# Optimization experiments

Hardware: AMD Instinct MI355X
Metric: run time of the kernel (lower is better)

Reference implementation:

```python
import jax, jax.numpy as jnp
import numpy as np

# SMPL-like kinematic tree parents for 21 body joints (child j -> parent index in the 22-slot feature)
KTREE_PARENTS = jnp.array([0, 0, 0, 1, 2, 3, 4, 5, 6, 7, 8, 9, 9, 9, 12, 13, 14, 16, 17, 18, 19], dtype=jnp.int32)
# np.linspace(22, 64, 3, endpoint=False, dtype=int)[::-1] for num_tokens=64, token_size_div=3, num_joints+1=22
UP_SIZES = [50, 36, 22]
NUM_JOINTS_P1 = 22


def conv1d_rep(x, w, b):
    # x: (B, Cin, L), w: (Cout, Cin, 3), replicate padding of 1 on each side
    xp = jnp.pad(x, ((0, 0), (0, 0), (1, 1)), mode='edge')
    y = jax.lax.conv_general_dilated(xp, w, (1,), 'VALID', dimension_numbers=('NCH', 'OIH', 'NCH'))
    return y + b[None, :, None]


def interp_linear(x, out_size):
    # torch nn.Upsample(mode='linear', align_corners=False) semantics; x: (B, C, L)
    L = x.shape[-1]
    coords = (jnp.arange(out_size, dtype=x.dtype) + 0.5) * (L / out_size) - 0.5
    coords = jnp.clip(coords, 0.0, L - 1)
    lo = jnp.floor(coords).astype(jnp.int32)
    hi = jnp.minimum(lo + 1, L - 1)
    w = coords - lo.astype(x.dtype)
    return x[..., lo] * (1.0 - w) + x[..., hi] * w


def rotation_6d_to_matrix(d6):
    # pytorch3d convention: rows b1, b2, b3 stacked at dim=-2
    a1, a2 = d6[..., :3], d6[..., 3:]
    b1 = a1 / jnp.linalg.norm(a1, axis=-1, keepdims=True)
    a2p = a2 - jnp.sum(b1 * a2, axis=-1, keepdims=True) * b1
    b2 = a2p / jnp.linalg.norm(a2p, axis=-1, keepdims=True)
    b3 = jnp.cross(b1, b2)
    return jnp.stack([b1, b2, b3], axis=-2)


def setup_inputs() -> dict:
    key = jax.random.key(0)
    ks = jax.random.split(key, 8)
    B, T, C, W, J, D = 1024, 64, 512, 512, 21, 6
    s = 0.02
    f32 = jnp.float32
    return {
        'x': jax.random.normal(ks[0], (B, T, C), f32),
        'conv1_w': jax.random.normal(ks[1], (W, C, 3), f32) * s,
        'conv1_b': jnp.zeros((W,), f32),
        'tok_w': jax.random.normal(ks[2], (T, T), f32) * s,
        'tok_b': jnp.zeros((T,), f32),
        'up_w': jax.random.normal(ks[3], (3, W, W, 3), f32) * s,
        'up_b': jnp.zeros((3, W), f32),
        'ln_g': jnp.ones((W,), f32),
        'ln_b': jnp.zeros((W,), f32),
        'beta_w': jax.random.normal(ks[4], (W, 10), f32) * s,
        'beta_b': jnp.zeros((10,), f32),
        'pw1': jax.random.normal(ks[5], (J, 2 * W, W), f32) * s,
        'pb1': jnp.zeros((J, W), f32),
        'pw2': jax.random.normal(ks[6], (J, W, D), f32) * s,
        'pb2': jax.random.normal(ks[7], (J, D), f32) * 0.1,
    }


def reference(x, conv1_w, conv1_b, tok_w, tok_b, up_w, up_b, ln_g, ln_b,
              beta_w, beta_b, pw1, pb1, pw2, pb2):
    # ---- decoder ----
    h = x.transpose(0, 2, 1)                                   # (B, C, T)
    h = jax.nn.relu(conv1d_rep(h, conv1_w, conv1_b))            # (B, W, T)
    # Conv1d(T, T, 1) applied on token axis (after permutes) == matmul over tokens
    h = jax.nn.relu(jnp.einsum('st,bwt->bws', tok_w, h) + tok_b[None, None, :])  # (B, W, T)
    for i, sz in enumerate(UP_SIZES):
        h = conv1d_rep(interp_linear(h, sz), up_w[i], up_b[i])
        if sz != NUM_JOINTS_P1:
            h = jax.nn.relu(h)
    # h: (B, W, 22)
    m = h.mean(axis=-1)                                         # (B, W)
    mu = m.mean(-1, keepdims=True)
    var = m.var(-1, keepdims=True)
    pred_beta = ((m - mu) / jnp.sqrt(var + 1e-5) * ln_g + ln_b) @ beta_w + beta_b  # (B, 10)
    jf = h.transpose(0, 2, 1)                                   # (B, 22, W)
    curr = jf[:, 1:, :]                                         # joint j+1 feats, (B, 21, W)
    parent = jf[:, KTREE_PARENTS, :]                            # parent feats,   (B, 21, W)
    feat = jnp.concatenate([curr, parent], axis=-1)             # (B, 21, 2W)
    hid = jax.nn.relu(jnp.einsum('bjc,jch->bjh', feat, pw1) + pb1[None])
    pose6d = jnp.einsum('bjh,jhd->bjd', hid, pw2) + pb2[None]   # (B, 21, 6)
    rotmat = rotation_6d_to_matrix(pose6d)                      # (B, 21, 3, 3)
    return pose6d, rotmat, pred_beta
```

## Files before the change

### kernel.cpp

```cpp
#include <hip/hip_runtime.h>


typedef unsigned short u16;
typedef unsigned short u16x4 __attribute__((ext_vector_type(4)));
typedef unsigned short u16x8 __attribute__((ext_vector_type(8)));
typedef float f32x4 __attribute__((ext_vector_type(4)));
typedef __bf16 bf16x8 __attribute__((ext_vector_type(8)));

__constant__ int KPAR_C[21] = {0,0,0,1,2,3,4,5,6,7,8,9,9,9,12,13,14,16,17,18,19};

__device__ __forceinline__ u16 bf16rne(float v) {
  unsigned b = __builtin_bit_cast(unsigned, v);
  return (u16)((b + 0x7fffu + ((b >> 16) & 1u)) >> 16);
}
__device__ __forceinline__ float bf16tof(u16 h) {
  unsigned b = ((unsigned)h) << 16;
  return __builtin_bit_cast(float, b);
}
__device__ __forceinline__ f32x4 mfma16(u16x8 a, u16x8 b, f32x4 c) {
  return __builtin_amdgcn_mfma_f32_16x16x32_bf16(
      __builtin_bit_cast(bf16x8, a), __builtin_bit_cast(bf16x8, b), c, 0, 0, 0);
}
__device__ __forceinline__ int unpack_c(int p) {
  return (p & ~31) | (((p >> 3) & 3) << 2) | (p & 3) | ((p & 4) << 2);
}
__device__ __forceinline__ void gload_lds16(const void* g, void* l) {
  __builtin_amdgcn_global_load_lds((const __attribute__((address_space(1))) void*)g,
                                   (__attribute__((address_space(3))) void*)l, 16, 0, 0);
}

__global__ __launch_bounds__(256)
void kwprep(const float* __restrict__ conv1_w, const float* __restrict__ up_w,
            const float* __restrict__ tok_w, u16* __restrict__ WF, u16* __restrict__ TWF) {
  int idx = blockIdx.x * 256 + threadIdx.x;
  if (idx < 786432) {
    const int lane = idx & 63;
    int r = idx >> 6;
    const int nf = r & 15; r >>= 4;
    const int ks = r % 48; r /= 48;
    const int p = r & 1; r >>= 1;
    const int nh = r & 1;
    const int L = r >> 1;
    const float* Wsrc = (L == 0) ? conv1_w : (up_w + (size_t)(L - 1) * 786432);
    const int wcol = unpack_c(nh * 256 + nf * 16 + (lane & 15));
    u16x8 o;
#pragma unroll
    for (int e = 0; e < 8; ++e) {
      const int k = ks * 32 + ((lane >> 4) << 2) + (e & 3) + ((e >> 2) << 4);
      const int c = k & 511, kk = k >> 9;
      const float v = Wsrc[(size_t)wcol * 1536 + c * 3 + kk];
      const u16 h = bf16rne(v);
      o[e] = p ? bf16rne(v - bf16tof(h)) : h;
    }
    *(u16x8*)(WF + (size_t)idx * 8) = o;
  } else if (idx < 786432 + 1024) {
    const int i2 = idx - 786432;
    const int lane = i2 & 63;
    const int r = i2 >> 6;
    const int mf = r & 3;
    const int ks = (r >> 2) & 1;
    const int p = r >> 3;
    const int s = mf * 16 + (lane & 15);
    u16x8 o;
#pragma unroll
    for (int e = 0; e < 8; ++e) {
      const int t = ks * 32 + ((lane >> 4) << 2) + (e & 3) + ((e >> 2) << 4);
      const float v = tok_w[s * 64 + t];
      const u16 h = bf16rne(v);
      o[e] = p ? bf16rne(v - bf16tof(h)) : h;
    }
    *(u16x8*)(TWF + (size_t)i2 * 8) = o;
  }
}

__global__ __launch_bounds__(256)
void kpw1prep(const float* __restrict__ pw1, u16* __restrict__ PWF) {
  const int idx = blockIdx.x * 256 + threadIdx.x;
  if (idx >= 2752512) return;
  const int lane = idx & 63;
  const int nf = (idx >> 6) & 15;
  const int ks = (idx >> 10) & 31;
  const int p = (idx >> 15) & 1;
  const int nh = (idx >> 16) & 1;
  const int j = idx >> 17;
  const int w = unpack_c(nh * 256 + nf * 16 + (lane & 15));
  u16x8 o;
#pragma unroll
  for (int e = 0; e < 8; ++e) {
    const int k = ks * 32 + ((lane >> 4) << 2) + (e & 3) + ((e >> 2) << 4);
    const float v = pw1[((size_t)j * 1024 + k) * 512 + w];
    const u16 h = bf16rne(v);
    o[e] = p ? bf16rne(v - bf16tof(h)) : h;
  }
  *(u16x8*)(PWF + (size_t)idx * 8) = o;
}

template <int SLOT, int ROWS, bool SRCF32, bool F32OUT, bool RELU>
__global__ __launch_bounds__(512, 2)
void conv_gemm(const float* __restrict__ xf,
               const u16* __restrict__ ghi, const u16* __restrict__ glo,
               const u16* __restrict__ wl,
               const float* __restrict__ bias,
               u16* __restrict__ ohi, u16* __restrict__ olo,
               float* __restrict__ of32) {
  constexpr int MFW = SLOT / 16;
  constexpr int MFT = 4 * MFW;
  constexpr int ASL = (MFT + 7) / 8;
  __shared__ u16x8 Ald[2][2][MFT][64];
  __shared__ u16x8 Bld[2][2][16][64];

  const int tid = threadIdx.x, lane = tid & 63, w = tid >> 6;
  const int mw = w & 3, nw = w >> 2;
  const int nh = blockIdx.x;
  const int bb0 = blockIdx.y * 4;

  f32x4 acc[MFW][8];
#pragma unroll
  for (int m = 0; m < MFW; ++m)
#pragma unroll
    for (int n = 0; n < 8; ++n) acc[m][n] = (f32x4){0.f, 0.f, 0.f, 0.f};

  float4 sF0[ASL], sF1[ASL];

  auto STAGE = [&](int ks2, int nb) {
    if constexpr (!SRCF32) {
      const int kk2 = ks2 >> 4;
      const int pc0 = (ks2 & 15) * 32 + ((lane >> 4) << 3);
#pragma unroll
      for (int si = 0; si < ASL; ++si) {
        const int f = w + si * 8;
        if (f < MFT) {
          const int bA = f / MFW, mfA = f % MFW;
          int t = mfA * 16 + (lane & 15) - 1 + kk2;
          t = t < 0 ? 0 : (t > ROWS - 1 ? ROWS - 1 : t);
          const size_t o = ((size_t)(bb0 + bA) * ROWS + t) * 512 + pc0;
          gload_lds16(ghi + o, &Ald[nb][0][f][0]);
          gload_lds16(glo + o, &Ald[nb][1][f][0]);
        }
      }
    }
#pragma unroll
    for (int ci = 0; ci < 4; ++ci) {
      const int cch = w + ci * 8;
      const int p = cch >> 4, nf = cch & 15;
      gload_lds16(wl + ((size_t)(((nh * 2 + p) * 48 + ks2) * 16 + nf)) * 512 + lane * 8,
                  &Bld[nb][p][nf][0]);
    }
  };

  auto LOADSA = [&](int ks2) {
    const int kk2 = ks2 >> 4;
    const int c0 = (ks2 & 15) * 32 + ((lane >> 4) << 2);
#pragma unroll
    for (int si = 0; si < ASL; ++si) {
      const int f = w + si * 8;
      if (f < MFT) {
        const int bA = f / MFW, mfA = f % MFW;
        int t = mfA * 16 + (lane & 15) - 1 + kk2;
        t = t < 0 ? 0 : (t > ROWS - 1 ? ROWS - 1 : t);
        const float* src = xf + ((size_t)(bb0 + bA) * ROWS + t) * 512 + c0;
        sF0[si] = *(const float4*)src;
        sF1[si] = *(const float4*)(src + 16);
      }
    }
  };
  auto WRITESA = [&](int nb) {
#pragma unroll
    for (int si = 0; si < ASL; ++si) {
      const int f = w + si * 8;
      if (f < MFT) {
        float vv[8] = {sF0[si].x, sF0[si].y, sF0[si].z, sF0[si].w,
                       sF1[si].x, sF1[si].y, sF1[si].z, sF1[si].w};
        u16x8 hv, lv;
#pragma unroll
        for (int e = 0; e < 8; ++e) {
          const u16 h = bf16rne(vv[e]);
          hv[e] = h;
          lv[e] = bf16rne(vv[e] - bf16tof(h));
        }
        Ald[nb][0][f][lane] = hv;
        Ald[nb][1][f][lane] = lv;
      }
    }
  };

  STAGE(0, 0);
  if constexpr (SRCF32) { LOADSA(0); WRITESA(0); }
  __syncthreads();

  for (int ks = 0; ks < 48; ++ks) {
    const int buf = ks & 1;
    if (ks < 47) {
      STAGE(ks + 1, buf ^ 1);
      if constexpr (SRCF32) LOADSA(ks + 1);
    }
    u16x8 ah[MFW], al[MFW];
#pragma unroll
    for (int m = 0; m < MFW; ++m) {
      ah[m] = Ald[buf][0][mw * MFW + m][lane];
      al[m] = Ald[buf][1][mw * MFW + m][lane];
    }
    __builtin_amdgcn_s_setprio(1);
#pragma unroll
    for (int n = 0; n < 8; ++n) {
      const u16x8 bh = Bld[buf][0][nw * 8 + n][lane];
      const u16x8 bl = Bld[buf][1][nw * 8 + n][lane];
#pragma unroll
      for (int m = 0; m < MFW; ++m) {
        acc[m][n] = mfma16(ah[m], bh, acc[m][n]);
        acc[m][n] = mfma16(ah[m], bl, acc[m][n]);
        acc[m][n] = mfma16(al[m], bh, acc[m][n]);
      }
    }
    __builtin_amdgcn_s_setprio(0);
    if (ks < 47) {
      if constexpr (SRCF32) WRITESA(buf ^ 1);
    }
    __syncthreads();
  }

  const int b = bb0 + mw;
#pragma unroll
  for (int m = 0; m < MFW; ++m) {
#pragma unroll
    for (int n = 0; n < 8; ++n) {
      const int col = nh * 256 + nw * 128 + n * 16 + (lane & 15);
      const float bs = bias[unpack_c(col)];
#pragma unroll
      for (int r = 0; r < 4; ++r) {
        const int t = m * 16 + ((lane >> 4) << 2) + r;
        if (t < ROWS) {
          float v = acc[m][n][r] + bs;
          if (RELU) v = fmaxf(v, 0.f);
          const size_t o = ((size_t)b * ROWS + t) * 512 + col;
          if constexpr (F32OUT) {
            of32[o] = v;
          } else {
            const u16 h = bf16rne(v);
            ohi[o] = h;
            olo[o] = bf16rne(v - bf16tof(h));
          }
        }
      }
    }
  }
}

__global__ __launch_bounds__(512, 2)
void tok_mix(const u16* __restrict__ h1hi, const u16* __restrict__ h1lo,
             const u16* __restrict__ twf, const float* __restrict__ tok_b,
             u16* __restrict__ g1hi, u16* __restrict__ g1lo) {
  __shared__ float h1f[64][258];
  __shared__ u16x8 twl[2][2][4][64];
  __shared__ float tbl[64];
  const int tid = threadIdx.x, lane = tid & 63, w = tid >> 6;
  const int mw = w & 3, nw = w >> 2;
  const int b = blockIdx.y, ch = blockIdx.x;

  for (int i = tid; i < 1024; i += 512) ((u16x8*)twl)[i] = ((const u16x8*)twf)[i];
  if (tid < 64) tbl[tid] = tok_b[tid];
  for (int i = tid; i < 2048; i += 512) {
    const int t = i >> 5, c8 = (i & 31) * 8;
    const size_t o = ((size_t)b * 64 + t) * 512 + ch * 256 + c8;
    const u16x8 hv = *(const u16x8*)(h1hi + o);
    const u16x8 lv = *(const u16x8*)(h1lo + o);
#pragma unroll
    for (int e = 0; e < 8; ++e) h1f[t][c8 + e] = bf16tof(hv[e]) + bf16tof(lv[e]);
  }
  __syncthreads();

  f32x4 acc2[8];
#pragma unroll
  for (int n = 0; n < 8; ++n) acc2[n] = (f32x4){0.f, 0.f, 0.f, 0.f};
#pragma unroll
  for (int ksI = 0; ksI < 2; ++ksI) {
    const u16x8 ah = twl[0][ksI][mw][lane];
    const u16x8 al = twl[1][ksI][mw][lane];
    const int t0 = ksI * 32 + ((lane >> 4) << 2);
#pragma unroll
    for (int n = 0; n < 8; ++n) {
      const int c = nw * 128 + n * 16 + (lane & 15);
      u16x8 bh, bl;
#pragma unroll
      for (int e = 0; e < 8; ++e) {
        const float v = h1f[t0 + (e & 3) + ((e >> 2) << 4)][c];
        const u16 h = bf16rne(v);
        bh[e] = h;
        bl[e] = bf16rne(v - bf16tof(h));
      }
      acc2[n] = mfma16(ah, bh, acc2[n]);
      acc2[n] = mfma16(ah, bl, acc2[n]);
      acc2[n] = mfma16(al, bh, acc2[n]);
    }
  }
  __syncthreads();
#pragma unroll
  for (int n = 0; n < 8; ++n) {
    const int c = nw * 128 + n * 16 + (lane & 15);
#pragma unroll
    for (int r = 0; r < 4; ++r) {
      const int s = mw * 16 + ((lane >> 4) << 2) + r;
      h1f[s][c] = fmaxf(acc2[n][r] + tbl[s], 0.f);
    }
  }
  __syncthreads();
  const float scale = (float)(64.0 / 50.0);
  for (int i = tid; i < 50 * 256; i += 512) {
    const int s = i >> 8, c = i & 255;
    float coords = fminf(fmaxf(((float)s + 0.5f) * scale - 0.5f, 0.f), 63.f);
    const int lo = (int)floorf(coords);
    const int hi = lo + 1 < 64 ? lo + 1 : 63;
    const float wv = coords - (float)lo;
    const float v = h1f[lo][c] * (1.f - wv) + h1f[hi][c] * wv;
    const u16 h = bf16rne(v);
    const size_t o = ((size_t)b * 50 + s) * 512 + ch * 256 + c;
    g1hi[o] = h;
    g1lo[o] = bf16rne(v - bf16tof(h));
  }
}

template <int SOUT, int SIN>
__global__ __launch_bounds__(256)
void ginterp(const u16* __restrict__ ahi, const u16* __restrict__ alo,
             u16* __restrict__ ghi, u16* __restrict__ glo) {
  const int idx = blockIdx.x * 256 + threadIdx.x;
  if (idx >= 1024 * SOUT * 64) return;
  const int ch = (idx & 63) * 8;
  const int s = (idx >> 6) % SOUT;
  const int b = (idx >> 6) / SOUT;
  const float scale = (float)((double)SIN / (double)SOUT);
  float coords = fminf(fmaxf(((float)s + 0.5f) * scale - 0.5f, 0.f), (float)(SIN - 1));
  const int lo = (int)floorf(coords);
  const int hi = lo + 1 < SIN ? lo + 1 : SIN - 1;
  const float wv = coords - (float)lo;
  const size_t olo_ = ((size_t)b * SIN + lo) * 512 + ch;
  const size_t ohi_ = ((size_t)b * SIN + hi) * 512 + ch;
  const u16x8 vh0 = *(const u16x8*)(ahi + olo_), vl0 = *(const u16x8*)(alo + olo_);
  const u16x8 vh1 = *(const u16x8*)(ahi + ohi_), vl1 = *(const u16x8*)(alo + ohi_);
  u16x8 oh, ol;
#pragma unroll
  for (int e = 0; e < 8; ++e) {
    const float v0 = bf16tof(vh0[e]) + bf16tof(vl0[e]);
    const float v1 = bf16tof(vh1[e]) + bf16tof(vl1[e]);
    const float v = v0 * (1.f - wv) + v1 * wv;
    const u16 h = bf16rne(v);
    oh[e] = h;
    ol[e] = bf16rne(v - bf16tof(h));
  }
  const size_t oo = ((size_t)b * SOUT + s) * 512 + ch;
  *(u16x8*)(ghi + oo) = oh;
  *(u16x8*)(glo + oo) = ol;
}

__global__ __launch_bounds__(256)
void k_beta(const float* __restrict__ h, const float* __restrict__ ln_g,
            const float* __restrict__ ln_b, const float* __restrict__ beta_w,
            const float* __restrict__ beta_b, float* __restrict__ out) {
  __shared__ float nbuf[512];
  __shared__ float red[32];
  __shared__ float part[160];
  const int tid = threadIdx.x;
  const int b = blockIdx.x;
  const float* hb = h + (size_t)b * (22 * 512);
  float m0 = 0.f, m1 = 0.f;
  for (int t = 0; t < 22; ++t) {
    m0 += hb[t * 512 + tid];
    m1 += hb[t * 512 + tid + 256];
  }
  m0 *= (1.f / 22.f);
  m1 *= (1.f / 22.f);
  float s = m0 + m1, sq = m0 * m0 + m1 * m1;
  for (int off = 32; off > 0; off >>= 1) {
    s += __shfl_down(s, off);
    sq += __shfl_down(sq, off);
  }
  const int lane = tid & 63, wid = tid >> 6;
  if (lane == 0) { red[wid] = s; red[8 + wid] = sq; }
  __syncthreads();
  if (tid == 0) {
    float S = red[0] + red[1] + red[2] + red[3];
    float Q = red[8] + red[9] + red[10] + red[11];
    float mu = S * (1.f / 512.f);
    float var = Q * (1.f / 512.f) - mu * mu;
    red[16] = mu;
    red[17] = 1.f / sqrtf(var + 1e-5f);
  }
  __syncthreads();
  const float mu = red[16], rs = red[17];
  const int uc = unpack_c(tid);
  nbuf[tid] = (m0 - mu) * rs * ln_g[uc] + ln_b[uc];
  nbuf[tid + 256] = (m1 - mu) * rs * ln_g[uc + 256] + ln_b[uc + 256];
  __syncthreads();
  if (tid < 160) {
    const int o = tid >> 4, l = tid & 15;
    float p = 0.f;
    for (int w = l; w < 512; w += 16) p += nbuf[w] * beta_w[unpack_c(w) * 10 + o];
    part[tid] = p;
  }
  __syncthreads();
  if (tid < 10) {
    float p = beta_b[tid];
#pragma unroll
    for (int l = 0; l < 16; ++l) p += part[tid * 16 + l];
    out[(size_t)b * 10 + tid] = p;
  }
}

__global__ __launch_bounds__(512, 2)
void k_pose1(const float* __restrict__ hf, const u16* __restrict__ PWF,
             const float* __restrict__ pb1,
             u16* __restrict__ hidhi, u16* __restrict__ hidlo) {
  __shared__ u16x8 Ald[2][2][8][64];
  __shared__ u16x8 Bld[2][2][16][64];
  const int tid = threadIdx.x, lane = tid & 63, w = tid >> 6;
  const int mw = w & 1, nw = w >> 1;
  const int nh = blockIdx.x & 1, mb = blockIdx.x >> 1;
  const int j = blockIdx.y;
  const int bb0 = mb * 128;
  const int par = KPAR_C[j];
  const size_t pwbase = (size_t)(j * 2 + nh) * 524288;

  f32x4 acc[4][4];
#pragma unroll
  for (int m = 0; m < 4; ++m)
#pragma unroll
    for (int n = 0; n < 4; ++n) acc[m][n] = (f32x4){0.f, 0.f, 0.f, 0.f};

  float4 sF0, sF1;

  auto STAGE = [&](int ks, int nb) {
#pragma unroll
    for (int t = 0; t < 4; ++t) {
      const int cc = t * 8 + w;
      const int p = cc >> 4, nf = cc & 15;
      gload_lds16(PWF + pwbase + ((size_t)(p * 32 + ks) * 16 + nf) * 512 + lane * 8,
                  &Bld[nb][p][nf][0]);
    }
  };
  auto LOADSA = [&](int ks) {
    const int row = (ks < 16) ? (j + 1) : par;
    const int b = bb0 + w * 16 + (lane & 15);
    const int pc0 = (ks & 15) * 32 + ((lane >> 4) << 3);
    const float* src = hf + ((size_t)b * 22 + row) * 512 + pc0;
    sF0 = *(const float4*)src;
    sF1 = *(const float4*)(src + 4);
  };
  auto WRITESA = [&](int nb) {
    float vv[8] = {sF0.x, sF0.y, sF0.z, sF0.w, sF1.x, sF1.y, sF1.z, sF1.w};
    u16x8 hv, lv;
#pragma unroll
    for (int e = 0; e < 8; ++e) {
      const u16 h = bf16rne(vv[e]);
      hv[e] = h;
      lv[e] = bf16rne(vv[e] - bf16tof(h));
    }
    Ald[nb][0][w][lane] = hv;
    Ald[nb][1][w][lane] = lv;
  };

  STAGE(0, 0);
  LOADSA(0);
  WRITESA(0);
  __syncthreads();

  for (int ks = 0; ks < 32; ++ks) {
    const int buf = ks & 1;
    if (ks < 31) { STAGE(ks + 1, buf ^ 1); LOADSA(ks + 1); }
    u16x8 ah[4], al[4], bh[4], bl[4];
#pragma unroll
    for (int m = 0; m < 4; ++m) {
      ah[m] = Ald[buf][0][mw * 4 + m][lane];
      al[m] = Ald[buf][1][mw * 4 + m][lane];
    }
#pragma unroll
    for (int n = 0; n < 4; ++n) {
      bh[n] = Bld[buf][0][nw * 4 + n][lane];
      bl[n] = Bld[buf][1][nw * 4 + n][lane];
    }
    __builtin_amdgcn_s_setprio(1);
#pragma unroll
    for (int n = 0; n < 4; ++n)
#pragma unroll
      for (int m = 0; m < 4; ++m) {
        acc[m][n] = mfma16(ah[m], bh[n], acc[m][n]);
        acc[m][n] = mfma16(ah[m], bl[n], acc[m][n]);
        acc[m][n] = mfma16(al[m], bh[n], acc[m][n]);
      }
    __builtin_amdgcn_s_setprio(0);
    if (ks < 31) WRITESA(buf ^ 1);
    __syncthreads();
  }

#pragma unroll
  for (int m = 0; m < 4; ++m) {
#pragma unroll
    for (int n = 0; n < 4; ++n) {
      const int col = nh * 256 + nw * 64 + n * 16 + (lane & 15);
      const float bs = pb1[(size_t)j * 512 + unpack_c(col)];
#pragma unroll
      for (int r = 0; r < 4; ++r) {
        const int b = bb0 + mw * 64 + m * 16 + ((lane >> 4) << 2) + r;
        float v = fmaxf(acc[m][n][r] + bs, 0.f);
        const size_t o = ((size_t)j * 1024 + b) * 512 + col;
        const u16 h = bf16rne(v);
        hidhi[o] = h;
        hidlo[o] = bf16rne(v - bf16tof(h));
      }
    }
  }
}

__global__ __launch_bounds__(256)
void k_pose2(const u16* __restrict__ hidhi, const u16* __restrict__ hidlo,
             const float* __restrict__ pw2, const float* __restrict__ pb2,
             float* __restrict__ out) {
  __shared__ float w2l[3072];
  __shared__ float part[128 * 12];
  const int tid = threadIdx.x;
  const int mb = blockIdx.x, j = blockIdx.y;
  const int bb0 = mb * 128;
  for (int i = tid; i < 3072; i += 256) {
    const int p = i / 6, d = i - p * 6;
    w2l[i] = pw2[(size_t)j * 3072 + unpack_c(p) * 6 + d];
  }
  __syncthreads();

  const int r = tid >> 1, half = tid & 1;
  const int row = bb0 + r;
  const u16* ph = hidhi + ((size_t)j * 1024 + row) * 512 + half * 256;
  const u16* pl = hidlo + ((size_t)j * 1024 + row) * 512 + half * 256;
  float s[6] = {0.f, 0.f, 0.f, 0.f, 0.f, 0.f};
  for (int c = 0; c < 32; ++c) {
    const u16x8 hv = ((const u16x8*)ph)[c];
    const u16x8 lv = ((const u16x8*)pl)[c];
#pragma unroll
    for (int e = 0; e < 8; ++e) {
      const float v = bf16tof(hv[e]) + bf16tof(lv[e]);
      const int hidx = half * 256 + c * 8 + e;
#pragma unroll
      for (int d = 0; d < 6; ++d) s[d] = fmaf(v, w2l[hidx * 6 + d], s[d]);
    }
  }
#pragma unroll
  for (int d = 0; d < 6; ++d) part[r * 12 + half * 6 + d] = s[d];
  __syncthreads();

  if (tid < 128) {
    const int row2 = bb0 + tid;
    float p6[6];
#pragma unroll
    for (int d = 0; d < 6; ++d)
      p6[d] = part[tid * 12 + d] + part[tid * 12 + 6 + d] + pb2[j * 6 + d];
    float* po = out + ((size_t)row2 * 21 + j) * 6;
#pragma unroll
    for (int d = 0; d < 6; ++d) po[d] = p6[d];
    const float a1x = p6[0], a1y = p6[1], a1z = p6[2];
    const float a2x = p6[3], a2y = p6[4], a2z = p6[5];
    const float inv1 = 1.f / sqrtf(a1x * a1x + a1y * a1y + a1z * a1z);
    const float b1x = a1x * inv1, b1y = a1y * inv1, b1z = a1z * inv1;
    const float dot = b1x * a2x + b1y * a2y + b1z * a2z;
    const float px = a2x - dot * b1x, py = a2y - dot * b1y, pz = a2z - dot * b1z;
    const float inv2 = 1.f / sqrtf(px * px + py * py + pz * pz);
    const float b2x = px * inv2, b2y = py * inv2, b2z = pz * inv2;
    const float b3x = b1y * b2z - b1z * b2y;
    const float b3y = b1z * b2x - b1x * b2z;
    const float b3z = b1x * b2y - b1y * b2x;
    float* ro = out + 129024 + ((size_t)row2 * 21 + j) * 9;
    ro[0] = b1x; ro[1] = b1y; ro[2] = b1z;
    ro[3] = b2x; ro[4] = b2y; ro[5] = b2z;
    ro[6] = b3x; ro[7] = b3y; ro[8] = b3z;
  }
}

extern "C" void kernel_launch(void* const* d_in, const int* in_sizes, int n_in,
                              void* d_out, int out_size, void* d_ws, size_t ws_size,
                              hipStream_t stream) {
  (void)in_sizes; (void)n_in; (void)out_size; (void)ws_size;
  const float* x       = (const float*)d_in[0];
  const float* conv1_w = (const float*)d_in[1];
  const float* conv1_b = (const float*)d_in[2];
  const float* tok_w   = (const float*)d_in[3];
  const float* tok_b   = (const float*)d_in[4];
  const float* up_w    = (const float*)d_in[5];
  const float* up_b    = (const float*)d_in[6];
  const float* ln_g    = (const float*)d_in[7];
  const float* ln_b    = (const float*)d_in[8];
  const float* beta_w  = (const float*)d_in[9];
  const float* beta_b  = (const float*)d_in[10];
  const float* pw1     = (const float*)d_in[11];
  const float* pb1     = (const float*)d_in[12];
  const float* pw2     = (const float*)d_in[13];
  const float* pb2     = (const float*)d_in[14];
  float* outp = (float*)d_out;

  char* base = (char*)d_ws;
  u16* WF  = (u16*)base;
  u16* TWF = WF + 6291456;
  u16* PA16 = (u16*)(base + 12599296);
  u16* PB16 = (u16*)(base + 12599296 + 134217728);
  u16* h1hi = PA16;            u16* h1lo = PA16 + 33554432;
  u16* a2hi = PA16;            u16* a2lo = PA16 + 26214400;
  u16* a3hi = PA16;            u16* a3lo = PA16 + 18874368;
  float* hf = (float*)PA16;
  u16* g1hi = PB16;            u16* g1lo = PB16 + 26214400;
  u16* g2hi = PB16;            u16* g2lo = PB16 + 18874368;
  u16* g3hi = PB16;            u16* g3lo = PB16 + 11534336;
  u16* PWF   = PB16;
  u16* hidhi = PB16 + 22020096;
  u16* hidlo = PB16 + 33030144;

  const size_t WL = 1572864;

  kwprep<<<3076, 256, 0, stream>>>(conv1_w, up_w, tok_w, WF, TWF);
  conv_gemm<64, 64, true, false, true><<<dim3(2, 256), 512, 0, stream>>>(
      x, nullptr, nullptr, WF, conv1_b, h1hi, h1lo, nullptr);
  tok_mix<<<dim3(2, 1024), 512, 0, stream>>>(h1hi, h1lo, TWF, tok_b, g1hi, g1lo);
  conv_gemm<64, 50, false, false, true><<<dim3(2, 256), 512, 0, stream>>>(
      nullptr, g1hi, g1lo, WF + WL, up_b, a2hi, a2lo, nullptr);
  ginterp<36, 50><<<9216, 256, 0, stream>>>(a2hi, a2lo, g2hi, g2lo);
  conv_gemm<48, 36, false, false, true><<<dim3(2, 256), 512, 0, stream>>>(
      nullptr, g2hi, g2lo, WF + 2 * WL, up_b + 512, a3hi, a3lo, nullptr);
  ginterp<22, 36><<<5632, 256, 0, stream>>>(a3hi, a3lo, g3hi, g3lo);
  conv_gemm<32, 22, false, true, false><<<dim3(2, 256), 512, 0, stream>>>(
      nullptr, g3hi, g3lo, WF + 3 * WL, up_b + 1024, nullptr, nullptr, hf);
  kpw1prep<<<10752, 256, 0, stream>>>(pw1, PWF);
  k_pose1<<<dim3(16, 21), 512, 0, stream>>>(hf, PWF, pb1, hidhi, hidlo);
  k_beta<<<1024, 256, 0, stream>>>(hf, ln_g, ln_b, beta_w, beta_b, outp + 322560);
  k_pose2<<<dim3(8, 21), 256, 0, stream>>>(hidhi, hidlo, pw2, pb2, outp);
}
```

Measured before the change: 1.363 ms.

## Load conv activation rows once per channel slice and reuse across taps

The conv GEMM used to reload the A tile from global memory for each of the three kernel taps. It now stages ROWS+2 edge-clamped rows per 32-channel slice into an XOR-swizzled LDS buffer and reads the three shifted windows from there, reordering the K loop so the taps of a slice run back to back. This cuts global A traffic and the fp32-to-bf16 split work by about 3x, at the cost of more LDS, register staging in place of direct-to-LDS loads, and a changed double-buffer schedule. The grid is also swapped so batch blocks vary fastest, and k_pose1's block index mapping is changed, altering L2 locality for weights.

```diff
diff --git a/kernel.cpp b/kernel.cpp
--- a/kernel.cpp
+++ b/kernel.cpp
@@ -104,15 +104,16 @@
                u16* __restrict__ ohi, u16* __restrict__ olo,
                float* __restrict__ of32) {
   constexpr int MFW = SLOT / 16;
-  constexpr int MFT = 4 * MFW;
-  constexpr int ASL = (MFT + 7) / 8;
-  __shared__ u16x8 Ald[2][2][MFT][64];
+  constexpr int SP = ROWS + 2;
+  constexpr int TOT = 32 * SP;
+  constexpr int AIT = (TOT + 511) / 512;
+  __shared__ u16x8 Alin[2][2][4][SP][4];
   __shared__ u16x8 Bld[2][2][16][64];
 
   const int tid = threadIdx.x, lane = tid & 63, w = tid >> 6;
   const int mw = w & 3, nw = w >> 2;
-  const int nh = blockIdx.x;
-  const int bb0 = blockIdx.y * 4;
+  const int nh = blockIdx.y;
+  const int bb0 = blockIdx.x * 4;
 
   f32x4 acc[MFW][8];
 #pragma unroll
@@ -120,25 +121,60 @@
 #pragma unroll
     for (int n = 0; n < 8; ++n) acc[m][n] = (f32x4){0.f, 0.f, 0.f, 0.f};
 
-  float4 sF0[ASL], sF1[ASL];
-
-  auto STAGE = [&](int ks2, int nb) {
-    if constexpr (!SRCF32) {
-      const int kk2 = ks2 >> 4;
-      const int pc0 = (ks2 & 15) * 32 + ((lane >> 4) << 3);
-#pragma unroll
-      for (int si = 0; si < ASL; ++si) {
-        const int f = w + si * 8;
-        if (f < MFT) {
-          const int bA = f / MFW, mfA = f % MFW;
-          int t = mfA * 16 + (lane & 15) - 1 + kk2;
-          t = t < 0 ? 0 : (t > ROWS - 1 ? ROWS - 1 : t);
-          const size_t o = ((size_t)(bb0 + bA) * ROWS + t) * 512 + pc0;
-          gload_lds16(ghi + o, &Ald[nb][0][f][0]);
-          gload_lds16(glo + o, &Ald[nb][1][f][0]);
+  float4 rf[AIT];
+  u16x4 rh[AIT], rl[AIT];
+
+  auto ALOADg = [&](int cs1) {
+#pragma unroll
+    for (int it = 0; it < AIT; ++it) {
+      const int i = it * 512 + tid;
+      if (i < TOT) {
+        const int q = i & 7;
+        const int s = (i >> 3) % SP;
+        const int b = i / (8 * SP);
+        int row = s - 1;
+        row = row < 0 ? 0 : (row > ROWS - 1 ? ROWS - 1 : row);
+        if constexpr (SRCF32) {
+          const int ofs = ((q >> 1) << 2) | ((q & 1) << 4);
+          rf[it] = *(const float4*)(xf + ((size_t)(bb0 + b) * ROWS + row) * 512 +
+                                    cs1 * 32 + ofs);
+        } else {
+          const size_t o = ((size_t)(bb0 + b) * ROWS + row) * 512 + cs1 * 32 + q * 4;
+          rh[it] = *(const u16x4*)(ghi + o);
+          rl[it] = *(const u16x4*)(glo + o);
         }
       }
     }
+  };
+  auto AWRITE = [&](int dst) {
+#pragma unroll
+    for (int it = 0; it < AIT; ++it) {
+      const int i = it * 512 + tid;
+      if (i < TOT) {
+        const int q = i & 7;
+        const int s = (i >> 3) % SP;
+        const int b = i / (8 * SP);
+        const int ci = ((q >> 1) ^ ((s >> 1) & 3)) * 2 + (q & 1);
+        u16x4 hv, lv;
+        if constexpr (SRCF32) {
+          float vv[4] = {rf[it].x, rf[it].y, rf[it].z, rf[it].w};
+#pragma unroll
+          for (int e = 0; e < 4; ++e) {
+            const u16 h = bf16rne(vv[e]);
+            hv[e] = h;
+            lv[e] = bf16rne(vv[e] - bf16tof(h));
+          }
+        } else {
+          hv = rh[it];
+          lv = rl[it];
+        }
+        ((u16x4*)&Alin[dst][0][b][s][0])[ci] = hv;
+        ((u16x4*)&Alin[dst][1][b][s][0])[ci] = lv;
+      }
+    }
+  };
+  auto BSTAGE = [&](int u2, int nb) {
+    const int ks2 = (u2 % 3) * 16 + (u2 / 3);
 #pragma unroll
     for (int ci = 0; ci < 4; ++ci) {
       const int cch = w + ci * 8;
@@ -148,75 +184,44 @@
     }
   };
 
-  auto LOADSA = [&](int ks2) {
-    const int kk2 = ks2 >> 4;
-    const int c0 = (ks2 & 15) * 32 + ((lane >> 4) << 2);
-#pragma unroll
-    for (int si = 0; si < ASL; ++si) {
-      const int f = w + si * 8;
-      if (f < MFT) {
-        const int bA = f / MFW, mfA = f % MFW;
-        int t = mfA * 16 + (lane & 15) - 1 + kk2;
-        t = t < 0 ? 0 : (t > ROWS - 1 ? ROWS - 1 : t);
-        const float* src = xf + ((size_t)(bb0 + bA) * ROWS + t) * 512 + c0;
-        sF0[si] = *(const float4*)src;
-        sF1[si] = *(const float4*)(src + 16);
-      }
-    }
-  };
-  auto WRITESA = [&](int nb) {
-#pragma unroll
-    for (int si = 0; si < ASL; ++si) {
-      const int f = w + si * 8;
-      if (f < MFT) {
-        float vv[8] = {sF0[si].x, sF0[si].y, sF0[si].z, sF0[si].w,
-                       sF1[si].x, sF1[si].y, sF1[si].z, sF1[si].w};
-        u16x8 hv, lv;
-#pragma unroll
-        for (int e = 0; e < 8; ++e) {
-          const u16 h = bf16rne(vv[e]);
-          hv[e] = h;
-          lv[e] = bf16rne(vv[e] - bf16tof(h));
+  ALOADg(0);
+  AWRITE(0);
+  BSTAGE(0, 0);
+  __syncthreads();
+
+  for (int cs = 0; cs < 16; ++cs) {
+    const int ab = cs & 1;
+    for (int kk = 0; kk < 3; ++kk) {
+      const int u = cs * 3 + kk;
+      if (u < 47) BSTAGE(u + 1, (u + 1) & 1);
+      if (kk == 0 && cs < 15) ALOADg(cs + 1);
+      const int bbuf = u & 1;
+      u16x8 ah[MFW], al[MFW];
+#pragma unroll
+      for (int m = 0; m < MFW; ++m) {
+        const int t = m * 16 + (lane & 15);
+        int s = t + kk;
+        if (s > ROWS + 1) s = ROWS + 1;
+        const int cw = (lane >> 4) ^ ((s >> 1) & 3);
+        ah[m] = Alin[ab][0][mw][s][cw];
+        al[m] = Alin[ab][1][mw][s][cw];
+      }
+      __builtin_amdgcn_s_setprio(1);
+#pragma unroll
+      for (int n = 0; n < 8; ++n) {
+        const u16x8 bh = Bld[bbuf][0][nw * 8 + n][lane];
+        const u16x8 bl = Bld[bbuf][1][nw * 8 + n][lane];
+#pragma unroll
+        for (int m = 0; m < MFW; ++m) {
+          acc[m][n] = mfma16(ah[m], bh, acc[m][n]);
+          acc[m][n] = mfma16(ah[m], bl, acc[m][n]);
+          acc[m][n] = mfma16(al[m], bh, acc[m][n]);
         }
-        Ald[nb][0][f][lane] = hv;
-        Ald[nb][1][f][lane] = lv;
-      }
-    }
-  };
-
-  STAGE(0, 0);
-  if constexpr (SRCF32) { LOADSA(0); WRITESA(0); }
-  __syncthreads();
-
-  for (int ks = 0; ks < 48; ++ks) {
-    const int buf = ks & 1;
-    if (ks < 47) {
-      STAGE(ks + 1, buf ^ 1);
-      if constexpr (SRCF32) LOADSA(ks + 1);
-    }
-    u16x8 ah[MFW], al[MFW];
-#pragma unroll
-    for (int m = 0; m < MFW; ++m) {
-      ah[m] = Ald[buf][0][mw * MFW + m][lane];
-      al[m] = Ald[buf][1][mw * MFW + m][lane];
-    }
-    __builtin_amdgcn_s_setprio(1);
-#pragma unroll
-    for (int n = 0; n < 8; ++n) {
-      const u16x8 bh = Bld[buf][0][nw * 8 + n][lane];
-      const u16x8 bl = Bld[buf][1][nw * 8 + n][lane];
-#pragma unroll
-      for (int m = 0; m < MFW; ++m) {
-        acc[m][n] = mfma16(ah[m], bh, acc[m][n]);
-        acc[m][n] = mfma16(ah[m], bl, acc[m][n]);
-        acc[m][n] = mfma16(al[m], bh, acc[m][n]);
-      }
-    }
-    __builtin_amdgcn_s_setprio(0);
-    if (ks < 47) {
-      if constexpr (SRCF32) WRITESA(buf ^ 1);
-    }
-    __syncthreads();
+      }
+      __builtin_amdgcn_s_setprio(0);
+      if (kk == 1 && cs < 15) AWRITE(ab ^ 1);
+      __syncthreads();
+    }
   }
 
   const int b = bb0 + mw;
@@ -414,7 +419,7 @@
   __shared__ u16x8 Bld[2][2][16][64];
   const int tid = threadIdx.x, lane = tid & 63, w = tid >> 6;
   const int mw = w & 1, nw = w >> 1;
-  const int nh = blockIdx.x & 1, mb = blockIdx.x >> 1;
+  const int mb = blockIdx.x & 7, nh = blockIdx.x >> 3;
   const int j = blockIdx.y;
   const int bb0 = mb * 128;
   const int par = KPAR_C[j];
@@ -612,16 +617,16 @@
   const size_t WL = 1572864;
 
   kwprep<<<3076, 256, 0, stream>>>(conv1_w, up_w, tok_w, WF, TWF);
-  conv_gemm<64, 64, true, false, true><<<dim3(2, 256), 512, 0, stream>>>(
+  conv_gemm<64, 64, true, false, true><<<dim3(256, 2), 512, 0, stream>>>(
       x, nullptr, nullptr, WF, conv1_b, h1hi, h1lo, nullptr);
   tok_mix<<<dim3(2, 1024), 512, 0, stream>>>(h1hi, h1lo, TWF, tok_b, g1hi, g1lo);
-  conv_gemm<64, 50, false, false, true><<<dim3(2, 256), 512, 0, stream>>>(
+  conv_gemm<64, 50, false, false, true><<<dim3(256, 2), 512, 0, stream>>>(
       nullptr, g1hi, g1lo, WF + WL, up_b, a2hi, a2lo, nullptr);
   ginterp<36, 50><<<9216, 256, 0, stream>>>(a2hi, a2lo, g2hi, g2lo);
-  conv_gemm<48, 36, false, false, true><<<dim3(2, 256), 512, 0, stream>>>(
+  conv_gemm<48, 36, false, false, true><<<dim3(256, 2), 512, 0, stream>>>(
       nullptr, g2hi, g2lo, WF + 2 * WL, up_b + 512, a3hi, a3lo, nullptr);
   ginterp<22, 36><<<5632, 256, 0, stream>>>(a3hi, a3lo, g3hi, g3lo);
-  conv_gemm<32, 22, false, true, false><<<dim3(2, 256), 512, 0, stream>>>(
+  conv_gemm<32, 22, false, true, false><<<dim3(256, 2), 512, 0, stream>>>(
       nullptr, g3hi, g3lo, WF + 3 * WL, up_b + 1024, nullptr, nullptr, hf);
   kpw1prep<<<10752, 256, 0, stream>>>(pw1, PWF);
   k_pose1<<<dim3(16, 21), 512, 0, stream>>>(hf, PWF, pb1, hidhi, hidlo);
```

Result: slower. 1.689 ms (+23.9%).
